# Performance work log

Measured on AMD Instinct MI355X. Metric: run time of the kernel, lower is better.

Reference implementation:

```python
import jax, jax.numpy as jnp
import numpy as np

N_EMBED = 2048
N_HEAD = 16
HEAD_SIZE = N_EMBED // N_HEAD  # 128


def rotate_half(x):
    x1, x2 = jnp.split(x, 2, axis=-1)
    return jnp.concatenate((-x2, x1), axis=-1)


def setup_inputs() -> dict:
    key = jax.random.key(0)
    k_x, k_qkv, k_proj, k_b = jax.random.split(key, 4)
    B, T = 4, 2048
    x = jax.random.normal(k_x, (B, T, N_EMBED), dtype=jnp.float32)
    # weights stored as [in, out] so y = x @ W (equivalent param'n of nn.Linear)
    w_qkv = jax.random.normal(k_qkv, (N_EMBED, 3 * N_EMBED), dtype=jnp.float32) * (N_EMBED ** -0.5)
    w_proj = jax.random.normal(k_proj, (N_EMBED, N_EMBED), dtype=jnp.float32) * (N_EMBED ** -0.5)
    b_proj = jax.random.normal(k_b, (N_EMBED,), dtype=jnp.float32) * 0.02
    return {"x": x, "w_qkv": w_qkv, "w_proj": w_proj, "b_proj": b_proj}


def reference(x, w_qkv, w_proj, b_proj):
    B, T, C = x.shape
    H, D = N_HEAD, HEAD_SIZE
    qkv = x @ w_qkv                                   # [B,T,3C]
    q, k, v = jnp.split(qkv, 3, axis=2)
    q = q.reshape(B, T, H, D).transpose(0, 2, 1, 3)   # [B,H,T,D]
    k = k.reshape(B, T, H, D).transpose(0, 2, 1, 3)
    v = v.reshape(B, T, H, D).transpose(0, 2, 1, 3)
    # RoPE in fp32
    inv_freq = 1.0 / (10000.0 ** (jnp.arange(0, D, 2, dtype=jnp.float32) / D))
    t = jnp.arange(T, dtype=jnp.float32)
    freqs = jnp.einsum('i,j->ij', t, inv_freq)        # [T,D/2]
    emb = jnp.concatenate((freqs, freqs), axis=-1)    # [T,D]
    cos = jnp.cos(emb)[None, None, :, :]
    sin = jnp.sin(emb)[None, None, :, :]
    qf = q.astype(jnp.float32)
    kf = k.astype(jnp.float32)
    q = (qf * cos + rotate_half(qf) * sin).astype(v.dtype)
    k = (kf * cos + rotate_half(kf) * sin).astype(v.dtype)
    # causal SDPA
    scale = 1.0 / jnp.sqrt(jnp.asarray(D, dtype=q.dtype))
    scores = jnp.einsum('bhqd,bhkd->bhqk', q, k) * scale
    causal = jnp.tril(jnp.ones((T, T), dtype=bool))
    scores = jnp.where(causal[None, None, :, :], scores, jnp.finfo(scores.dtype).min)
    attn = jax.nn.softmax(scores, axis=-1)
    out = jnp.einsum('bhqk,bhkd->bhqd', attn, v)      # [B,H,T,D]
    out = out.transpose(0, 2, 1, 3).reshape(B, T, C)
    return out @ w_proj + b_proj
```

## Files before the change

### kernel.cpp

```cpp
#include <hip/hip_runtime.h>
#include <hip/hip_bf16.h>
#include <cstdint>
#include <cstddef>

typedef __bf16 bf16x8 __attribute__((ext_vector_type(8)));
typedef __bf16 bf16x4 __attribute__((ext_vector_type(4)));
typedef float  f32x4  __attribute__((ext_vector_type(4)));

__device__ __forceinline__ void lds_load16(const void* gsrc, void* ldst) {
    __builtin_amdgcn_global_load_lds(
        (const __attribute__((address_space(1))) unsigned int*)gsrc,
        (__attribute__((address_space(3))) unsigned int*)ldst,
        16, 0, 0);
}

__global__ __launch_bounds__(256) void cvt_k(const float* __restrict__ in,
                                             __bf16* __restrict__ out, int n8) {
    int i = blockIdx.x * 256 + threadIdx.x;
    if (i >= n8) return;
    const float4* p4 = (const float4*)in + (size_t)i * 2;
    float4 a = p4[0], b = p4[1];
    bf16x8 o;
    o[0] = (__bf16)a.x; o[1] = (__bf16)a.y; o[2] = (__bf16)a.z; o[3] = (__bf16)a.w;
    o[4] = (__bf16)b.x; o[5] = (__bf16)b.y; o[6] = (__bf16)b.z; o[7] = (__bf16)b.w;
    *((bf16x8*)out + i) = o;
}

__global__ __launch_bounds__(256) void transp_k(const float* __restrict__ W,
                                                __bf16* __restrict__ WT, int R, int C) {
    __shared__ float tile[32][33];
    int tx = threadIdx.x & 31, ty = threadIdx.x >> 5;
    int c0 = blockIdx.x * 32, r0 = blockIdx.y * 32;
#pragma unroll
    for (int k = 0; k < 4; ++k)
        tile[ty + 8 * k][tx] = W[(size_t)(r0 + ty + 8 * k) * C + c0 + tx];
    __syncthreads();
#pragma unroll
    for (int k = 0; k < 4; ++k)
        WT[(size_t)(c0 + ty + 8 * k) * R + r0 + tx] = (__bf16)tile[tx][ty + 8 * k];
}

__global__ __launch_bounds__(256) void sincos_k(float2* __restrict__ sc) {
    int idx = blockIdx.x * 256 + threadIdx.x;
    int t = idx >> 6, j = idx & 63;
    float inv = powf(10000.f, -(float)j / 64.f);
    float f = (float)t * inv;
    float s, c;
    sincosf(f, &s, &c);
    sc[idx] = make_float2(c, s);
}

__global__ __launch_bounds__(512, 2) void gemm8_k(const __bf16* __restrict__ A,
                                                  const __bf16* __restrict__ Bt,
                                                  int nbn, int mode,
                                                  __bf16* __restrict__ qb, __bf16* __restrict__ kb,
                                                  __bf16* __restrict__ vt,
                                                  float* __restrict__ outp,
                                                  const float* __restrict__ bias,
                                                  const float2* __restrict__ sc) {
    __shared__ __bf16 lds[2][2][2][128 * 64];
    const int K = 2048, NT = K / 64;
    int nwg = gridDim.x;
    int per = nwg >> 3;
    int bid = blockIdx.x;
    int wg = (bid & 7) * per + (bid >> 3);
    int bm = wg / nbn, bn = wg % nbn;
    int m0 = bm * 256, n0 = bn * 256;
    int tid = threadIdx.x;
    int lane = tid & 63, wave = tid >> 6;
    int wm = wave >> 2, wn = wave & 3;
    int lr = lane & 15, lg = lane >> 4;

    f32x4 acc[8][4] = {};

    auto stageA = [&](int db, int sub, int kt) {
#pragma unroll
        for (int l = 0; l < 2; ++l) {
            int chunk = l * 512 + tid;
            int r = chunk >> 3, c16 = chunk & 7;
            int rg = m0 + ((r >> 6) << 7) + (sub << 6) + (r & 63);
            lds_load16(A + (size_t)rg * K + (kt << 6) + ((c16 ^ (r & 7)) << 3),
                       &lds[db][0][sub][chunk * 8]);
        }
    };
    auto stageB = [&](int db, int sub, int kt) {
#pragma unroll
        for (int l = 0; l < 2; ++l) {
            int chunk = l * 512 + tid;
            int r = chunk >> 3, c16 = chunk & 7;
            int rg = n0 + ((r >> 5) << 6) + (sub << 5) + (r & 31);
            lds_load16(Bt + (size_t)rg * K + (kt << 6) + ((c16 ^ (r & 7)) << 3),
                       &lds[db][1][sub][chunk * 8]);
        }
    };
    auto rdA = [&](int db, int sub, int q, int kk) -> bf16x8 {
        int r = (wm << 6) + (q << 4) + lr;
        int cb = ((kk << 6) + (lg << 4)) ^ ((r & 7) << 4);
        return *(const bf16x8*)((const char*)&lds[db][0][sub][0] + r * 128 + cb);
    };
    auto rdB = [&](int db, int j, int kk) -> bf16x8 {
        int sub = j >> 1;
        int r = (wn << 5) + ((j & 1) << 4) + lr;
        int cb = ((kk << 6) + (lg << 4)) ^ ((r & 7) << 4);
        return *(const bf16x8*)((const char*)&lds[db][1][sub][0] + r * 128 + cb);
    };

    stageA(0, 0, 0); stageB(0, 0, 0); stageB(0, 1, 0); stageA(0, 1, 0);
    asm volatile("s_waitcnt vmcnt(4)" ::: "memory");
    __builtin_amdgcn_s_barrier();

    bf16x8 a[4][2], bA[2][2], bB[2][2];
    for (int t = 0; t < NT; ++t) {
        int db = t & 1, dn = db ^ 1;
        bool pf = (t + 1 < NT);
#pragma unroll
        for (int q = 0; q < 4; ++q) { a[q][0] = rdA(db, 0, q, 0); a[q][1] = rdA(db, 0, q, 1); }
#pragma unroll
        for (int j = 0; j < 2; ++j) { bA[j][0] = rdB(db, j, 0); bA[j][1] = rdB(db, j, 1); }
        if (pf) stageA(dn, 0, t + 1);
        __builtin_amdgcn_s_barrier();
        asm volatile("s_waitcnt lgkmcnt(0)" ::: "memory");
        __builtin_amdgcn_sched_barrier(0);
        __builtin_amdgcn_s_setprio(1);
#pragma unroll
        for (int q = 0; q < 4; ++q)
#pragma unroll
            for (int j = 0; j < 2; ++j)
#pragma unroll
                for (int kk = 0; kk < 2; ++kk)
                    acc[q][j] = __builtin_amdgcn_mfma_f32_16x16x32_bf16(a[q][kk], bA[j][kk], acc[q][j], 0, 0, 0);
        __builtin_amdgcn_s_setprio(0);
        if (pf) asm volatile("s_waitcnt vmcnt(4)" ::: "memory");
        else    asm volatile("s_waitcnt vmcnt(2)" ::: "memory");
        __builtin_amdgcn_s_barrier();
#pragma unroll
        for (int j = 0; j < 2; ++j) { bB[j][0] = rdB(db, j + 2, 0); bB[j][1] = rdB(db, j + 2, 1); }
        if (pf) stageB(dn, 0, t + 1);
        __builtin_amdgcn_s_barrier();
        asm volatile("s_waitcnt lgkmcnt(0)" ::: "memory");
        __builtin_amdgcn_sched_barrier(0);
        __builtin_amdgcn_s_setprio(1);
#pragma unroll
        for (int q = 0; q < 4; ++q)
#pragma unroll
            for (int j = 0; j < 2; ++j)
#pragma unroll
                for (int kk = 0; kk < 2; ++kk)
                    acc[q][j + 2] = __builtin_amdgcn_mfma_f32_16x16x32_bf16(a[q][kk], bB[j][kk], acc[q][j + 2], 0, 0, 0);
        __builtin_amdgcn_s_setprio(0);
        if (pf) asm volatile("s_waitcnt vmcnt(4)" ::: "memory");
        else    asm volatile("s_waitcnt vmcnt(0)" ::: "memory");
        __builtin_amdgcn_s_barrier();
#pragma unroll
        for (int q = 0; q < 4; ++q) { a[q][0] = rdA(db, 1, q, 0); a[q][1] = rdA(db, 1, q, 1); }
        if (pf) stageB(dn, 1, t + 1);
        __builtin_amdgcn_s_barrier();
        asm volatile("s_waitcnt lgkmcnt(0)" ::: "memory");
        __builtin_amdgcn_sched_barrier(0);
        __builtin_amdgcn_s_setprio(1);
#pragma unroll
        for (int q = 0; q < 4; ++q)
#pragma unroll
            for (int j = 0; j < 2; ++j)
#pragma unroll
                for (int kk = 0; kk < 2; ++kk)
                    acc[q + 4][j + 2] = __builtin_amdgcn_mfma_f32_16x16x32_bf16(a[q][kk], bB[j][kk], acc[q + 4][j + 2], 0, 0, 0);
        __builtin_amdgcn_s_setprio(0);
        __builtin_amdgcn_s_barrier();
        if (pf) stageA(dn, 1, t + 1);
        __builtin_amdgcn_s_setprio(1);
#pragma unroll
        for (int q = 0; q < 4; ++q)
#pragma unroll
            for (int j = 0; j < 2; ++j)
#pragma unroll
                for (int kk = 0; kk < 2; ++kk)
                    acc[q + 4][j] = __builtin_amdgcn_mfma_f32_16x16x32_bf16(a[q][kk], bA[j][kk], acc[q + 4][j], 0, 0, 0);
        __builtin_amdgcn_s_setprio(0);
        if (pf) asm volatile("s_waitcnt vmcnt(4)" ::: "memory");
        __builtin_amdgcn_s_barrier();
    }

    if (mode == 0) {
        int which = n0 >> 11;
        if (which == 2) {
#pragma unroll
            for (int q = 0; q < 8; ++q) {
                int row_t = (wm << 7) + ((q >> 2) << 6) + ((q & 3) << 4) + (lg << 2);
#pragma unroll
                for (int j = 0; j < 4; ++j) {
                    int c = n0 + (wn << 6) + (j << 4) + lr;
                    int h = (c & 2047) >> 7, d = c & 127;
#pragma unroll
                    for (int r = 0; r < 4; ++r) {
                        int row = m0 + row_t + r;
                        int b_ = row >> 11, tt = row & 2047;
                        vt[((size_t)(b_ * 16 + h) * 128 + d) * 2048 + tt] = (__bf16)acc[q][j][r];
                    }
                }
            }
        } else {
            __bf16* dst = (which == 0) ? qb : kb;
            float scale = (which == 0) ? 0.08838834764831845f : 1.f;
            float* scr = (float*)&lds[0][0][0][0];
            int rl = (wm << 4) + (lg << 2);
            int colw = (wn << 6);
#pragma unroll
            for (int q = 0; q < 8; ++q) {
                int row_t = (wm << 7) + ((q >> 2) << 6) + ((q & 3) << 4) + (lg << 2);
#pragma unroll
                for (int j = 0; j < 4; ++j)
#pragma unroll
                    for (int r = 0; r < 4; ++r)
                        scr[(rl + r) * 260 + colw + (j << 4) + lr] = acc[q][j][r];
                __syncthreads();
#pragma unroll
                for (int j = 0; j < 4; ++j) {
                    int c = n0 + colw + (j << 4) + lr;
                    int h = (c & 2047) >> 7, d = c & 127;
                    int jj = (j << 4) + lr;
#pragma unroll
                    for (int r = 0; r < 4; ++r) {
                        int row = m0 + row_t + r;
                        int b_ = row >> 11, tt = row & 2047;
                        float2 cs = sc[tt * 64 + jj];
                        float v0 = acc[q][j][r];
                        float v1 = scr[(rl + r) * 260 + (colw ^ 64) + (j << 4) + lr];
                        float o = ((wn & 1) == 0) ? (v0 * cs.x - v1 * cs.y)
                                                  : (v0 * cs.x + v1 * cs.y);
                        dst[((size_t)(b_ * 16 + h) * 2048 + tt) * 128 + d] = (__bf16)(o * scale);
                    }
                }
                __syncthreads();
            }
        }
    } else {
#pragma unroll
        for (int q = 0; q < 8; ++q) {
            int row_t = (wm << 7) + ((q >> 2) << 6) + ((q & 3) << 4) + (lg << 2);
#pragma unroll
            for (int j = 0; j < 4; ++j) {
                int col = n0 + (wn << 6) + (j << 4) + lr;
                float bv = bias[col];
#pragma unroll
                for (int r = 0; r < 4; ++r) {
                    int row = m0 + row_t + r;
                    outp[(size_t)row * 2048 + col] = acc[q][j][r] + bv;
                }
            }
        }
    }
}

__global__ __launch_bounds__(256, 2) void attn_k(const __bf16* __restrict__ qb,
                                                 const __bf16* __restrict__ kb,
                                                 const __bf16* __restrict__ vt,
                                                 __bf16* __restrict__ ao) {
    __shared__ __bf16 Ks[64 * 128];
    __shared__ __bf16 Vs[128 * 64];
    __shared__ __bf16 Ps[4][16 * 64];

    int bid = blockIdx.x;
    int qt = 31 - (bid >> 6);
    int bh = bid & 63;
    int qs = qt * 64;
    int tid = threadIdx.x, wave = tid >> 6, lane = tid & 63;
    int lr = lane & 15, lg = lane >> 4;

    bf16x8 qf[4];
    const __bf16* Qrow = qb + ((size_t)bh * 2048 + qs + wave * 16 + lr) * 128;
#pragma unroll
    for (int kk = 0; kk < 4; ++kk) qf[kk] = *(const bf16x8*)(Qrow + kk * 32 + lg * 8);

    f32x4 ot[8] = {};
    float m_run = -1e30f, l_run = 0.f;

    for (int ks = 0; ks <= qs; ks += 64) {
#pragma unroll
        for (int i = 0; i < 4; ++i) {
            int c = tid + i * 256;
            {
                int row = c >> 4;
                int cc = c ^ (row & 7);
                int dd = (cc & 15) * 8;
                lds_load16(kb + ((size_t)bh * 2048 + ks + row) * 128 + dd, Ks + c * 8);
            }
            {
                int row = c >> 3;
                int cc = c ^ (row & 7);
                int tt = (cc & 7) * 8;
                lds_load16(vt + ((size_t)bh * 128 + row) * 2048 + ks + tt, Vs + c * 8);
            }
        }
        __syncthreads();

        f32x4 st[4];
        __builtin_amdgcn_s_setprio(1);
#pragma unroll
        for (int mt = 0; mt < 4; ++mt) {
            f32x4 s = {};
#pragma unroll
            for (int kk = 0; kk < 4; ++kk) {
                int row = mt * 16 + lr;
                const __bf16* kp = Ks + row * 128 + ((((kk * 64 + lg * 16)) ^ ((row & 7) << 4)) >> 1);
                bf16x8 afr = *(const bf16x8*)kp;
                s = __builtin_amdgcn_mfma_f32_16x16x32_bf16(afr, qf[kk], s, 0, 0, 0);
            }
            st[mt] = s;
        }
        __builtin_amdgcn_s_setprio(0);

        if (ks == qs) {
            int q = qs + wave * 16 + lr;
#pragma unroll
            for (int mt = 0; mt < 4; ++mt)
#pragma unroll
                for (int r = 0; r < 4; ++r) {
                    int kv = ks + mt * 16 + lg * 4 + r;
                    if (kv > q) st[mt][r] = -1e30f;
                }
        }

        float pm = -1e30f;
#pragma unroll
        for (int mt = 0; mt < 4; ++mt)
#pragma unroll
            for (int r = 0; r < 4; ++r) pm = fmaxf(pm, st[mt][r]);
        pm = fmaxf(pm, __shfl_xor(pm, 16));
        pm = fmaxf(pm, __shfl_xor(pm, 32));
        float nm = fmaxf(m_run, pm);
        float alpha = __expf(m_run - nm);
        float psum = 0.f;
#pragma unroll
        for (int mt = 0; mt < 4; ++mt)
#pragma unroll
            for (int r = 0; r < 4; ++r) {
                float p = __expf(st[mt][r] - nm);
                psum += p;
                st[mt][r] = p;
            }
        psum += __shfl_xor(psum, 16);
        psum += __shfl_xor(psum, 32);
        l_run = l_run * alpha + psum;
        m_run = nm;
#pragma unroll
        for (int t8 = 0; t8 < 8; ++t8) ot[t8] *= alpha;

#pragma unroll
        for (int mt = 0; mt < 4; ++mt) {
            bf16x4 pk;
#pragma unroll
            for (int r = 0; r < 4; ++r) pk[r] = (__bf16)st[mt][r];
            int byteoff = lr * 128 + (((mt * 32 + lg * 8)) ^ ((lr & 7) << 4));
            *(bf16x4*)((char*)&Ps[wave][0] + byteoff) = pk;
        }

        bf16x8 pfr[2];
#pragma unroll
        for (int kk = 0; kk < 2; ++kk) {
            const char* pp = (const char*)&Ps[wave][0] + lr * 128 + (((kk * 64 + lg * 16)) ^ ((lr & 7) << 4));
            pfr[kk] = *(const bf16x8*)pp;
        }
        __builtin_amdgcn_s_setprio(1);
#pragma unroll
        for (int dt = 0; dt < 8; ++dt) {
#pragma unroll
            for (int kk = 0; kk < 2; ++kk) {
                int row = dt * 16 + lr;
                const __bf16* vp = Vs + row * 64 + ((((kk * 64 + lg * 16)) ^ ((row & 7) << 4)) >> 1);
                bf16x8 afr = *(const bf16x8*)vp;
                ot[dt] = __builtin_amdgcn_mfma_f32_16x16x32_bf16(afr, pfr[kk], ot[dt], 0, 0, 0);
            }
        }
        __builtin_amdgcn_s_setprio(0);
        __syncthreads();
    }

    float inv = 1.f / l_run;
    int b_ = bh >> 4, h = bh & 15;
    size_t rowbase = ((size_t)b_ * 2048 + qs + wave * 16 + lr) * 2048 + h * 128;
#pragma unroll
    for (int dt = 0; dt < 8; ++dt) {
        bf16x4 o;
#pragma unroll
        for (int r = 0; r < 4; ++r) o[r] = (__bf16)(ot[dt][r] * inv);
        *(bf16x4*)(ao + rowbase + dt * 16 + lg * 4) = o;
    }
}

extern "C" void kernel_launch(void* const* d_in, const int* in_sizes, int n_in,
                              void* d_out, int out_size, void* d_ws, size_t ws_size,
                              hipStream_t stream) {
    const float* x      = (const float*)d_in[0];
    const float* w_qkv  = (const float*)d_in[1];
    const float* w_proj = (const float*)d_in[2];
    const float* b_proj = (const float*)d_in[3];
    float* out = (float*)d_out;
    char* ws = (char*)d_ws;

    __bf16* xb  = (__bf16*)(ws);
    __bf16* wqt = (__bf16*)(ws + 33554432);
    __bf16* wpt = (__bf16*)(ws + 58720256);
    __bf16* qb  = (__bf16*)(ws + 67108864);
    __bf16* kb  = (__bf16*)(ws + 100663296);
    __bf16* vt  = (__bf16*)(ws + 134217728);
    __bf16* ao  = (__bf16*)(ws + 167772160);
    float2* sc  = (float2*)(ws + 201326592);

    hipLaunchKernelGGL(cvt_k, dim3(8192), dim3(256), 0, stream, x, xb, 2097152);
    hipLaunchKernelGGL(transp_k, dim3(192, 64), dim3(256), 0, stream, w_qkv, wqt, 2048, 6144);
    hipLaunchKernelGGL(transp_k, dim3(64, 64), dim3(256), 0, stream, w_proj, wpt, 2048, 2048);
    hipLaunchKernelGGL(sincos_k, dim3(512), dim3(256), 0, stream, sc);
    hipLaunchKernelGGL(gemm8_k, dim3(768), dim3(512), 0, stream,
                       xb, wqt, 24, 0, qb, kb, vt, (float*)nullptr, (const float*)nullptr, sc);
    hipLaunchKernelGGL(attn_k, dim3(2048), dim3(256), 0, stream, qb, kb, vt, ao);
    hipLaunchKernelGGL(gemm8_k, dim3(256), dim3(512), 0, stream,
                       ao, wpt, 8, 1, (__bf16*)nullptr, (__bf16*)nullptr, (__bf16*)nullptr,
                       out, b_proj, (const float2*)nullptr);
}
```

Measured before the change: 407.7 us.

## Double attention query tile per block and vectorize QKV epilogue stores

```diff
diff --git a/kernel.cpp b/kernel.cpp
--- a/kernel.cpp
+++ b/kernel.cpp
@@ -191,12 +191,12 @@
                 for (int j = 0; j < 4; ++j) {
                     int c = n0 + (wn << 6) + (j << 4) + lr;
                     int h = (c & 2047) >> 7, d = c & 127;
-#pragma unroll
-                    for (int r = 0; r < 4; ++r) {
-                        int row = m0 + row_t + r;
-                        int b_ = row >> 11, tt = row & 2047;
-                        vt[((size_t)(b_ * 16 + h) * 128 + d) * 2048 + tt] = (__bf16)acc[q][j][r];
-                    }
+                    int row = m0 + row_t;
+                    int b_ = row >> 11, tt = row & 2047;
+                    bf16x4 o;
+#pragma unroll
+                    for (int r = 0; r < 4; ++r) o[r] = (__bf16)acc[q][j][r];
+                    *(bf16x4*)(vt + ((size_t)(b_ * 16 + h) * 128 + d) * 2048 + tt) = o;
                 }
             }
         } else {
@@ -205,32 +205,34 @@
             float* scr = (float*)&lds[0][0][0][0];
             int rl = (wm << 4) + (lg << 2);
             int colw = (wn << 6);
-#pragma unroll
-            for (int q = 0; q < 8; ++q) {
-                int row_t = (wm << 7) + ((q >> 2) << 6) + ((q & 3) << 4) + (lg << 2);
+            int srow = tid & 31;
+            int scol = (tid >> 5) << 4;
+#pragma unroll
+            for (int q8 = 0; q8 < 8; ++q8) {
 #pragma unroll
                 for (int j = 0; j < 4; ++j)
 #pragma unroll
                     for (int r = 0; r < 4; ++r)
-                        scr[(rl + r) * 260 + colw + (j << 4) + lr] = acc[q][j][r];
+                        scr[(rl + r) * 257 + colw + (j << 4) + lr] = acc[q8][j][r];
                 __syncthreads();
-#pragma unroll
-                for (int j = 0; j < 4; ++j) {
-                    int c = n0 + colw + (j << 4) + lr;
-                    int h = (c & 2047) >> 7, d = c & 127;
-                    int jj = (j << 4) + lr;
-#pragma unroll
-                    for (int r = 0; r < 4; ++r) {
-                        int row = m0 + row_t + r;
-                        int b_ = row >> 11, tt = row & 2047;
-                        float2 cs = sc[tt * 64 + jj];
-                        float v0 = acc[q][j][r];
-                        float v1 = scr[(rl + r) * 260 + (colw ^ 64) + (j << 4) + lr];
-                        float o = ((wn & 1) == 0) ? (v0 * cs.x - v1 * cs.y)
-                                                  : (v0 * cs.x + v1 * cs.y);
-                        dst[((size_t)(b_ * 16 + h) * 2048 + tt) * 128 + d] = (__bf16)(o * scale);
-                    }
-                }
+                int grow = m0 + ((srow >> 4) << 7) + ((q8 >> 2) << 6) + ((q8 & 3) << 4) + (srow & 15);
+                int b_ = grow >> 11, tt = grow & 2047;
+                bf16x8 o8[2];
+#pragma unroll
+                for (int e = 0; e < 16; ++e) {
+                    int cc = scol + e;
+                    float v0 = scr[srow * 257 + cc];
+                    float v1 = scr[srow * 257 + (cc ^ 64)];
+                    float2 cs = sc[tt * 64 + (cc & 63)];
+                    float o = ((cc & 64) == 0) ? (v0 * cs.x - v1 * cs.y)
+                                               : (v0 * cs.x + v1 * cs.y);
+                    o8[e >> 3][e & 7] = (__bf16)(o * scale);
+                }
+                int c0 = n0 + scol;
+                int h = (c0 >> 7) & 15, d = c0 & 127;
+                __bf16* dp = dst + ((size_t)(b_ * 16 + h) * 2048 + tt) * 128 + d;
+                *(bf16x8*)dp = o8[0];
+                *(bf16x8*)(dp + 8) = o8[1];
                 __syncthreads();
             }
         }
@@ -252,18 +254,18 @@
     }
 }
 
-__global__ __launch_bounds__(256, 2) void attn_k(const __bf16* __restrict__ qb,
+__global__ __launch_bounds__(512, 2) void attn_k(const __bf16* __restrict__ qb,
                                                  const __bf16* __restrict__ kb,
                                                  const __bf16* __restrict__ vt,
                                                  __bf16* __restrict__ ao) {
     __shared__ __bf16 Ks[64 * 128];
     __shared__ __bf16 Vs[128 * 64];
-    __shared__ __bf16 Ps[4][16 * 64];
+    __shared__ __bf16 Ps[8][16 * 64];
 
     int bid = blockIdx.x;
-    int qt = 31 - (bid >> 6);
+    int qt = 15 - (bid >> 6);
     int bh = bid & 63;
-    int qs = qt * 64;
+    int qs = qt * 128;
     int tid = threadIdx.x, wave = tid >> 6, lane = tid & 63;
     int lr = lane & 15, lg = lane >> 4;
 
@@ -274,11 +276,13 @@
 
     f32x4 ot[8] = {};
     float m_run = -1e30f, l_run = 0.f;
-
-    for (int ks = 0; ks <= qs; ks += 64) {
-#pragma unroll
-        for (int i = 0; i < 4; ++i) {
-            int c = tid + i * 256;
+    int qmax = qs + wave * 16 + 15;
+    int kend = qs + 64;
+
+    for (int ks = 0; ks <= kend; ks += 64) {
+#pragma unroll
+        for (int i = 0; i < 2; ++i) {
+            int c = tid + i * 512;
             {
                 int row = c >> 4;
                 int cc = c ^ (row & 7);
@@ -294,85 +298,87 @@
         }
         __syncthreads();
 
-        f32x4 st[4];
-        __builtin_amdgcn_s_setprio(1);
-#pragma unroll
-        for (int mt = 0; mt < 4; ++mt) {
-            f32x4 s = {};
-#pragma unroll
-            for (int kk = 0; kk < 4; ++kk) {
-                int row = mt * 16 + lr;
-                const __bf16* kp = Ks + row * 128 + ((((kk * 64 + lg * 16)) ^ ((row & 7) << 4)) >> 1);
-                bf16x8 afr = *(const bf16x8*)kp;
-                s = __builtin_amdgcn_mfma_f32_16x16x32_bf16(afr, qf[kk], s, 0, 0, 0);
-            }
-            st[mt] = s;
-        }
-        __builtin_amdgcn_s_setprio(0);
-
-        if (ks == qs) {
-            int q = qs + wave * 16 + lr;
+        if (ks <= qmax) {
+            f32x4 st[4];
+            __builtin_amdgcn_s_setprio(1);
+#pragma unroll
+            for (int mt = 0; mt < 4; ++mt) {
+                f32x4 s = {};
+#pragma unroll
+                for (int kk = 0; kk < 4; ++kk) {
+                    int row = mt * 16 + lr;
+                    const __bf16* kp = Ks + row * 128 + ((((kk * 64 + lg * 16)) ^ ((row & 7) << 4)) >> 1);
+                    bf16x8 afr = *(const bf16x8*)kp;
+                    s = __builtin_amdgcn_mfma_f32_16x16x32_bf16(afr, qf[kk], s, 0, 0, 0);
+                }
+                st[mt] = s;
+            }
+            __builtin_amdgcn_s_setprio(0);
+
+            if (ks + 63 > qs + wave * 16) {
+                int q = qs + wave * 16 + lr;
+#pragma unroll
+                for (int mt = 0; mt < 4; ++mt)
+#pragma unroll
+                    for (int r = 0; r < 4; ++r) {
+                        int kv = ks + mt * 16 + lg * 4 + r;
+                        if (kv > q) st[mt][r] = -1e30f;
+                    }
+            }
+
+            float pm = -1e30f;
 #pragma unroll
             for (int mt = 0; mt < 4; ++mt)
 #pragma unroll
+                for (int r = 0; r < 4; ++r) pm = fmaxf(pm, st[mt][r]);
+            pm = fmaxf(pm, __shfl_xor(pm, 16));
+            pm = fmaxf(pm, __shfl_xor(pm, 32));
+            float nm = fmaxf(m_run, pm);
+            float alpha = __expf(m_run - nm);
+            float psum = 0.f;
+#pragma unroll
+            for (int mt = 0; mt < 4; ++mt)
+#pragma unroll
                 for (int r = 0; r < 4; ++r) {
-                    int kv = ks + mt * 16 + lg * 4 + r;
-                    if (kv > q) st[mt][r] = -1e30f;
-                }
-        }
-
-        float pm = -1e30f;
-#pragma unroll
-        for (int mt = 0; mt < 4; ++mt)
-#pragma unroll
-            for (int r = 0; r < 4; ++r) pm = fmaxf(pm, st[mt][r]);
-        pm = fmaxf(pm, __shfl_xor(pm, 16));
-        pm = fmaxf(pm, __shfl_xor(pm, 32));
-        float nm = fmaxf(m_run, pm);
-        float alpha = __expf(m_run - nm);
-        float psum = 0.f;
-#pragma unroll
-        for (int mt = 0; mt < 4; ++mt)
-#pragma unroll
-            for (int r = 0; r < 4; ++r) {
-                float p = __expf(st[mt][r] - nm);
-                psum += p;
-                st[mt][r] = p;
-            }
-        psum += __shfl_xor(psum, 16);
-        psum += __shfl_xor(psum, 32);
-        l_run = l_run * alpha + psum;
-        m_run = nm;
-#pragma unroll
-        for (int t8 = 0; t8 < 8; ++t8) ot[t8] *= alpha;
-
-#pragma unroll
-        for (int mt = 0; mt < 4; ++mt) {
-            bf16x4 pk;
-#pragma unroll
-            for (int r = 0; r < 4; ++r) pk[r] = (__bf16)st[mt][r];
-            int byteoff = lr * 128 + (((mt * 32 + lg * 8)) ^ ((lr & 7) << 4));
-            *(bf16x4*)((char*)&Ps[wave][0] + byteoff) = pk;
-        }
-
-        bf16x8 pfr[2];
-#pragma unroll
-        for (int kk = 0; kk < 2; ++kk) {
-            const char* pp = (const char*)&Ps[wave][0] + lr * 128 + (((kk * 64 + lg * 16)) ^ ((lr & 7) << 4));
-            pfr[kk] = *(const bf16x8*)pp;
-        }
-        __builtin_amdgcn_s_setprio(1);
-#pragma unroll
-        for (int dt = 0; dt < 8; ++dt) {
+                    float p = __expf(st[mt][r] - nm);
+                    psum += p;
+                    st[mt][r] = p;
+                }
+            psum += __shfl_xor(psum, 16);
+            psum += __shfl_xor(psum, 32);
+            l_run = l_run * alpha + psum;
+            m_run = nm;
+#pragma unroll
+            for (int t8 = 0; t8 < 8; ++t8) ot[t8] *= alpha;
+
+#pragma unroll
+            for (int mt = 0; mt < 4; ++mt) {
+                bf16x4 pk;
+#pragma unroll
+                for (int r = 0; r < 4; ++r) pk[r] = (__bf16)st[mt][r];
+                int byteoff = lr * 128 + (((mt * 32 + lg * 8)) ^ ((lr & 7) << 4));
+                *(bf16x4*)((char*)&Ps[wave][0] + byteoff) = pk;
+            }
+
+            bf16x8 pfr[2];
 #pragma unroll
             for (int kk = 0; kk < 2; ++kk) {
-                int row = dt * 16 + lr;
-                const __bf16* vp = Vs + row * 64 + ((((kk * 64 + lg * 16)) ^ ((row & 7) << 4)) >> 1);
-                bf16x8 afr = *(const bf16x8*)vp;
-                ot[dt] = __builtin_amdgcn_mfma_f32_16x16x32_bf16(afr, pfr[kk], ot[dt], 0, 0, 0);
-            }
-        }
-        __builtin_amdgcn_s_setprio(0);
+                const char* pp = (const char*)&Ps[wave][0] + lr * 128 + (((kk * 64 + lg * 16)) ^ ((lr & 7) << 4));
+                pfr[kk] = *(const bf16x8*)pp;
+            }
+            __builtin_amdgcn_s_setprio(1);
+#pragma unroll
+            for (int dt = 0; dt < 8; ++dt) {
+#pragma unroll
+                for (int kk = 0; kk < 2; ++kk) {
+                    int row = dt * 16 + lr;
+                    const __bf16* vp = Vs + row * 64 + ((((kk * 64 + lg * 16)) ^ ((row & 7) << 4)) >> 1);
+                    bf16x8 afr = *(const bf16x8*)vp;
+                    ot[dt] = __builtin_amdgcn_mfma_f32_16x16x32_bf16(afr, pfr[kk], ot[dt], 0, 0, 0);
+                }
+            }
+            __builtin_amdgcn_s_setprio(0);
+        }
         __syncthreads();
     }
 
@@ -413,7 +419,7 @@
     hipLaunchKernelGGL(sincos_k, dim3(512), dim3(256), 0, stream, sc);
     hipLaunchKernelGGL(gemm8_k, dim3(768), dim3(512), 0, stream,
                        xb, wqt, 24, 0, qb, kb, vt, (float*)nullptr, (const float*)nullptr, sc);
-    hipLaunchKernelGGL(attn_k, dim3(2048), dim3(256), 0, stream, qb, kb, vt, ao);
+    hipLaunchKernelGGL(attn_k, dim3(1024), dim3(512), 0, stream, qb, kb, vt, ao);
     hipLaunchKernelGGL(gemm8_k, dim3(256), dim3(512), 0, stream,
                        ao, wpt, 8, 1, (__bf16*)nullptr, (__bf16*)nullptr, (__bf16*)nullptr,
                        out, b_proj, (const float2*)nullptr);
```

Measured after the change: 417.1 us. 1.02x slower.
